# Performance work log

Hardware: AMD Instinct MI355X
Metric: run time of the kernel (lower is better)

Reference implementation:

```python
import jax, jax.numpy as jnp
import numpy as np

D_MODEL = 256
N_HEADS = 8
N_LEVELS = 4
N_POINTS = 4
SHAPES = [(128, 128), (64, 64), (32, 32), (16, 16)]  # (H, W) per level


def _query_hw(Lq):
    h = int(Lq ** 0.5)
    w = Lq // h
    if h * w != Lq:
        facs = [(i, Lq // i) for i in range(1, int(Lq ** 0.5) + 1) if Lq % i == 0]
        h, w = min(facs, key=lambda t: abs(t[0] - t[1]))
    return h, w


def _grid_sample(img, grid):
    # img: [B, D, H, W]; grid: [B, Lq, P, 2] in [-1,1] (x, y)
    # bilinear, padding_mode='zeros', align_corners=False
    B, D, H, W = img.shape
    gx, gy = grid[..., 0], grid[..., 1]
    x = ((gx + 1.0) * W - 1.0) * 0.5
    y = ((gy + 1.0) * H - 1.0) * 0.5
    x0 = jnp.floor(x)
    y0 = jnp.floor(y)
    wx1 = x - x0
    wy1 = y - y0
    wx0 = 1.0 - wx1
    wy0 = 1.0 - wy1
    x0i = x0.astype(jnp.int32)
    y0i = y0.astype(jnp.int32)
    x1i = x0i + 1
    y1i = y0i + 1
    img_flat = img.reshape(B, D, H * W)

    def gather(yi, xi):
        valid = (xi >= 0) & (xi < W) & (yi >= 0) & (yi < H)
        idx = jnp.clip(yi, 0, H - 1) * W + jnp.clip(xi, 0, W - 1)  # [B,Lq,P]
        v = jnp.take_along_axis(img_flat, idx.reshape(B, 1, -1), axis=2)
        v = v.reshape(B, D, *yi.shape[1:])  # [B,D,Lq,P]
        return v * valid[:, None].astype(img.dtype)

    return (gather(y0i, x0i) * (wy0 * wx0)[:, None]
            + gather(y0i, x1i) * (wy0 * wx1)[:, None]
            + gather(y1i, x0i) * (wy1 * wx0)[:, None]
            + gather(y1i, x1i) * (wy1 * wx1)[:, None])


def _forward(query, input_flatten, spatial_shapes,
             W_off, b_off, W_attn, b_attn, W_val, b_val, W_out, b_out):
    N, Lq, C = query.shape
    M, L, P = N_HEADS, N_LEVELS, N_POINTS
    D = C // M
    shapes = np.asarray(spatial_shapes)  # static

    value = (input_flatten @ W_val + b_val).reshape(N, -1, M, D)
    off = (query @ W_off + b_off).reshape(N, Lq, M, L, P, 2)
    attn = jax.nn.softmax((query @ W_attn + b_attn).reshape(N, Lq, M, L * P), axis=-1)
    attn = attn.reshape(N, Lq, M, L, P)

    # normalized reference grid derived from Len_q (2D branch)
    qh, qw = _query_hw(Lq)
    ry, rx = jnp.meshgrid(jnp.linspace(0.5, qh - 0.5, qh) / qh,
                          jnp.linspace(0.5, qw - 0.5, qw) / qw, indexing='ij')
    ref = jnp.stack([rx.reshape(-1), ry.reshape(-1)], axis=-1)  # [Lq, 2] (x,y)
    norm = jnp.asarray(np.stack([shapes[:, 1], shapes[:, 0]], -1), jnp.float32)  # [L,2]=(W,H)
    loc = ref[None, :, None, None, None, :] + off / norm[None, None, None, :, None, :]
    grids = 2.0 * loc - 1.0  # [N,Lq,M,L,P,2]

    starts = np.concatenate([[0], np.cumsum(shapes[:, 0] * shapes[:, 1])])
    sampled = []
    for l in range(L):
        H, W = int(shapes[l, 0]), int(shapes[l, 1])
        v = value[:, starts[l]:starts[l + 1]]            # [N, H*W, M, D]
        v = v.transpose(0, 2, 3, 1).reshape(N * M, D, H, W)
        g = grids[:, :, :, l].transpose(0, 2, 1, 3, 4).reshape(N * M, Lq, P, 2)
        sampled.append(_grid_sample(v, g))               # [NM, D, Lq, P]

    vals = jnp.stack(sampled, axis=-2)                   # [NM, D, Lq, L, P]
    # faithful to original: values flattened (P, L)-major, weights (L, P)-major
    vals = vals.transpose(0, 1, 2, 4, 3).reshape(N * M, D, Lq, P * L)
    w = attn.transpose(0, 2, 1, 3, 4).reshape(N * M, 1, Lq, L * P)
    out = (vals * w).sum(-1).reshape(N, M * D, Lq).transpose(0, 2, 1)  # [N,Lq,C]
    return out @ W_out + b_out


def setup_inputs():
    key = jax.random.key(0)
    ks = jax.random.split(key, 12)
    N, Lq, C = 2, 16384, D_MODEL
    M, L, P = N_HEADS, N_LEVELS, N_POINTS
    Lin = sum(h * w for h, w in SHAPES)
    s = 0.02
    # sampling_offsets bias: original directional grid init
    thetas = np.arange(M, dtype=np.float32) * (2.0 * np.pi / M)
    gi = np.stack([np.cos(thetas), np.sin(thetas)], -1)
    gi = gi / np.abs(gi).max(-1, keepdims=True)
    gi = np.tile(gi.reshape(M, 1, 1, 2), (1, L, P, 1))
    for i in range(P):
        gi[:, :, i, :] *= (i + 1)
    inp = {
        'query': jax.random.normal(ks[0], (N, Lq, C), jnp.float32),
        'reference_points': jax.random.uniform(ks[1], (N, Lq, L, 2), jnp.float32),
        'input_flatten': jax.random.normal(ks[2], (N, Lin, C), jnp.float32),
        'spatial_shapes': jnp.array(SHAPES, jnp.int32),
        'level_start_index': jnp.array(np.concatenate([[0], np.cumsum([h * w for h, w in SHAPES[:-1]])]), jnp.int32),
        'W_off': jax.random.normal(ks[3], (C, M * L * P * 2), jnp.float32) * s,
        'b_off': jnp.asarray(gi.reshape(-1), jnp.float32),
        'W_attn': jax.random.normal(ks[4], (C, M * L * P), jnp.float32) * s,
        'b_attn': jnp.zeros((M * L * P,), jnp.float32),
        'W_val': jax.random.normal(ks[5], (C, C), jnp.float32) * (1.0 / np.sqrt(C)),
        'b_val': jnp.zeros((C,), jnp.float32),
        'W_out': jax.random.normal(ks[6], (C, C), jnp.float32) * (1.0 / np.sqrt(C)),
        'b_out': jnp.zeros((C,), jnp.float32),
    }
    return inp


def reference(query, reference_points, input_flatten, spatial_shapes, level_start_index,
              W_off, b_off, W_attn, b_attn, W_val, b_val, W_out, b_out):
    assert reference_points.shape[-1] == 2
    return _forward(query, input_flatten, spatial_shapes,
                    W_off, b_off, W_attn, b_attn, W_val, b_val, W_out, b_out)
```

## Files before the change

kernel.cpp:

```cpp
#include <hip/hip_runtime.h>
#include <math.h>

#define NB   2
#define LQ   16384
#define CDIM 256
#define MH   8
#define DH   32
#define LIN  21760

typedef __attribute__((ext_vector_type(8))) _Float16 f16x8;
typedef __attribute__((ext_vector_type(4))) _Float16 f16x4;
typedef __attribute__((ext_vector_type(4))) float    f32x4;

__device__ __forceinline__ void async16(const void* g, void* l) {
    __builtin_amdgcn_global_load_lds(
        (const __attribute__((address_space(1))) void*)g,
        (__attribute__((address_space(3))) void*)l,
        16, 0, 0);
}

__global__ __launch_bounds__(256) void split_f16_kernel(
    const float* __restrict__ in, _Float16* __restrict__ o, int n8)
{
    const int i = blockIdx.x * 256 + threadIdx.x;
    if (i >= n8) return;
    const float4 v0 = ((const float4*)in)[i * 2];
    const float4 v1 = ((const float4*)in)[i * 2 + 1];
    f16x8 h;
    h[0] = (_Float16)v0.x; h[1] = (_Float16)v0.y;
    h[2] = (_Float16)v0.z; h[3] = (_Float16)v0.w;
    h[4] = (_Float16)v1.x; h[5] = (_Float16)v1.y;
    h[6] = (_Float16)v1.z; h[7] = (_Float16)v1.w;
    ((f16x8*)o)[i] = h;
}

__global__ __launch_bounds__(256) void tsplit_f16_kernel(
    const float* __restrict__ W, _Float16* __restrict__ t, int N)
{
    const int i = blockIdx.x * 256 + threadIdx.x;
    if (i >= N * 256) return;
    const int nn = i >> 8;
    const int kk = i & 255;
    t[i] = (_Float16)W[kk * N + nn];
}

template <bool OUT_F16>
__global__ __launch_bounds__(256) void gemm_f16(
    const _Float16* __restrict__ A, const _Float16* __restrict__ Bt,
    const float* __restrict__ bias0, const float* __restrict__ bias1,
    void* __restrict__ C0, void* __restrict__ C1,
    int M, int N, int K, int N0)
{
    __shared__ _Float16 Ash[128 * 32];
    __shared__ _Float16 Bsh[128 * 32];

    const int tid  = threadIdx.x;
    const int wave = tid >> 6, lane = tid & 63;
    const int quad = lane >> 4, l16 = lane & 15;
    const int bm = blockIdx.y * 128;
    const int bn = blockIdx.x * 128;
    const int wrow = wave * 32;

    f32x4 acc[2][8] = {};

    const int s0 = tid,        row0 = s0 >> 2, kg0 = (s0 & 3) << 3;
    const int s1 = tid + 256,  row1 = s1 >> 2, kg1 = (s1 & 3) << 3;

    for (int k0 = 0; k0 < K; k0 += 32) {
        async16(A  + (size_t)(bm + row0) * K + k0 + kg0, Ash + s0 * 8);
        async16(A  + (size_t)(bm + row1) * K + k0 + kg1, Ash + s1 * 8);
        async16(Bt + (size_t)(bn + row0) * K + k0 + kg0, Bsh + s0 * 8);
        async16(Bt + (size_t)(bn + row1) * K + k0 + kg1, Bsh + s1 * 8);
        __syncthreads();

        f16x8 ah[2];
        #pragma unroll
        for (int r = 0; r < 2; ++r)
            ah[r] = *(const f16x8*)&Ash[(wrow + r * 16 + l16) * 32 + quad * 8];
        #pragma unroll
        for (int half = 0; half < 2; ++half) {
            f16x8 bh[4];
            #pragma unroll
            for (int c = 0; c < 4; ++c)
                bh[c] = *(const f16x8*)&Bsh[(half * 64 + c * 16 + l16) * 32 + quad * 8];
            #pragma unroll
            for (int r = 0; r < 2; ++r)
                #pragma unroll
                for (int c = 0; c < 4; ++c)
                    acc[r][half * 4 + c] = __builtin_amdgcn_mfma_f32_16x16x32_f16(
                        ah[r], bh[c], acc[r][half * 4 + c], 0, 0, 0);
        }
        __syncthreads();
    }

    void* Cb; const float* bb; int ldc, coff;
    if (bn < N0) { Cb = C0; bb = bias0; ldc = N0;     coff = 0;  }
    else         { Cb = C1; bb = bias1; ldc = N - N0; coff = N0; }
    #pragma unroll
    for (int c = 0; c < 8; ++c) {
        const int col = bn + c * 16 + l16 - coff;
        const float bia = bb[col];
        #pragma unroll
        for (int r = 0; r < 2; ++r)
            #pragma unroll
            for (int i = 0; i < 4; ++i) {
                const int rr = bm + wrow + r * 16 + quad * 4 + i;
                const float v = acc[r][c][i] + bia;
                if (OUT_F16) ((_Float16*)Cb)[(size_t)rr * ldc + col] = (_Float16)v;
                else         ((float*)Cb)[(size_t)rr * ldc + col] = v;
            }
    }
}

__global__ __launch_bounds__(256) void softmax16_kernel(float* __restrict__ a, int rows)
{
    const int r = blockIdx.x * 256 + threadIdx.x;
    if (r >= rows) return;
    float* row = a + (size_t)r * 16;
    float v[16];
    float4* rv = (float4*)row;
    #pragma unroll
    for (int i = 0; i < 4; ++i) *(float4*)&v[i * 4] = rv[i];
    float mx = v[0];
    #pragma unroll
    for (int i = 1; i < 16; ++i) mx = fmaxf(mx, v[i]);
    float s = 0.f;
    #pragma unroll
    for (int i = 0; i < 16; ++i) { v[i] = __expf(v[i] - mx); s += v[i]; }
    const float inv = 1.f / s;
    #pragma unroll
    for (int i = 0; i < 16; ++i) v[i] *= inv;
    #pragma unroll
    for (int i = 0; i < 4; ++i) rv[i] = *(float4*)&v[i * 4];
}

__global__ __launch_bounds__(256) void sample_kernel_v7(
    const _Float16* __restrict__ value,
    const float* __restrict__ off,
    const float* __restrict__ attn,
    _Float16* __restrict__ outv)
{
    __shared__ __align__(16) float lds_task[8][516];

    const int tid = threadIdx.x;
    const int qbase = blockIdx.x * 4;

    #pragma unroll
    for (int j = 0; j < 2; ++j) {
        const int t  = tid + 256 * j;
        const int q  = t >> 7;
        const int m  = (t >> 4) & 7;
        const int pt = t & 15;
        const int l  = pt >> 2;
        const int p  = pt & 3;
        const int qi = qbase + q;
        const int lq = qi & (LQ - 1);
        const int n  = qi >> 14;

        const int Hl = 128 >> l;
        const int STARTS[4] = {0, 16384, 20480, 21504};

        const float2 oxy = *(const float2*)&off[(size_t)qi * 256 + m * 32 + pt * 2];
        const float w    = attn[(size_t)qi * 128 + m * 16 + p * 4 + l];

        const float refx = ((lq & 127) + 0.5f) * (1.0f / 128.0f);
        const float refy = ((lq >> 7)  + 0.5f) * (1.0f / 128.0f);

        const float x = refx * (float)Hl + oxy.x - 0.5f;
        const float y = refy * (float)Hl + oxy.y - 0.5f;
        const float x0f = floorf(x), y0f = floorf(y);
        const int x0 = (int)x0f, y0 = (int)y0f;
        const int x1 = x0 + 1,  y1 = y0 + 1;
        const float fx = x - x0f, fy = y - y0f;
        const float gx = 1.f - fx, gy = 1.f - fy;

        const float vx0 = (x0 >= 0 && x0 < Hl) ? 1.f : 0.f;
        const float vx1 = (x1 >= 0 && x1 < Hl) ? 1.f : 0.f;
        const float vy0 = (y0 >= 0 && y0 < Hl) ? 1.f : 0.f;
        const float vy1 = (y1 >= 0 && y1 < Hl) ? 1.f : 0.f;

        const int x0c = min(max(x0, 0), Hl - 1);
        const int x1c = min(max(x1, 0), Hl - 1);
        const int y0c = min(max(y0, 0), Hl - 1);
        const int y1c = min(max(y1, 0), Hl - 1);

        const int base = (n * LIN + STARTS[l]) * 256 + m * 32;
        const int i00 = base + (y0c * Hl + x0c) * 256;
        const int i01 = base + (y0c * Hl + x1c) * 256;
        const int i10 = base + (y1c * Hl + x0c) * 256;
        const int i11 = base + (y1c * Hl + x1c) * 256;

        float4 wv;
        wv.x = w * gy * gx * vy0 * vx0;
        wv.y = w * gy * fx * vy0 * vx1;
        wv.z = w * fy * gx * vy1 * vx0;
        wv.w = w * fy * fx * vy1 * vx1;

        float* dst = &lds_task[m][(q * 16 + pt) * 8];
        *(float4*)dst = wv;
        int4 iv = {i00, i01, i10, i11};
        *(int4*)(dst + 4) = iv;
    }
    __syncthreads();

    const int q  = tid >> 6;
    const int m  = (tid >> 3) & 7;
    const int d4 = tid & 7;
    const int qi = qbase + q;

    const _Float16* vbase = value + d4 * 4;

    float4 acc = {0.f, 0.f, 0.f, 0.f};
    #pragma unroll
    for (int pt = 0; pt < 16; ++pt) {
        const float* td = &lds_task[m][(q * 16 + pt) * 8];
        const float4 wv = *(const float4*)td;
        const int4  iv = *(const int4*)(td + 4);
        const f16x4 v00 = *(const f16x4*)&vbase[iv.x];
        const f16x4 v01 = *(const f16x4*)&vbase[iv.y];
        const f16x4 v10 = *(const f16x4*)&vbase[iv.z];
        const f16x4 v11 = *(const f16x4*)&vbase[iv.w];
        acc.x += wv.x * (float)v00[0] + wv.y * (float)v01[0] + wv.z * (float)v10[0] + wv.w * (float)v11[0];
        acc.y += wv.x * (float)v00[1] + wv.y * (float)v01[1] + wv.z * (float)v10[1] + wv.w * (float)v11[1];
        acc.z += wv.x * (float)v00[2] + wv.y * (float)v01[2] + wv.z * (float)v10[2] + wv.w * (float)v11[2];
        acc.w += wv.x * (float)v00[3] + wv.y * (float)v01[3] + wv.z * (float)v10[3] + wv.w * (float)v11[3];
    }

    f16x4 o;
    o.x = (_Float16)acc.x; o.y = (_Float16)acc.y;
    o.z = (_Float16)acc.z; o.w = (_Float16)acc.w;
    *(f16x4*)&outv[(size_t)qi * 256 + m * 32 + d4 * 4] = o;
}

extern "C" void kernel_launch(void* const* d_in, const int* in_sizes, int n_in,
                              void* d_out, int out_size, void* d_ws, size_t ws_size,
                              hipStream_t stream)
{
    const float* query         = (const float*)d_in[0];
    const float* input_flatten = (const float*)d_in[2];
    const float* W_off  = (const float*)d_in[5];
    const float* b_off  = (const float*)d_in[6];
    const float* W_attn = (const float*)d_in[7];
    const float* b_attn = (const float*)d_in[8];
    const float* W_val  = (const float*)d_in[9];
    const float* b_val  = (const float*)d_in[10];
    const float* W_out  = (const float*)d_in[11];
    const float* b_out  = (const float*)d_in[12];
    float* out = (float*)d_out;

    char* w = (char*)d_ws;
    _Float16* IFf16 = (_Float16*)w;
    _Float16* Qf16  = (_Float16*)w;
    _Float16* Sf16  = (_Float16*)w;
    _Float16* value16 = (_Float16*)(w + 23068672);
    float*    attnbuf = (float*)(w + 67633152);
    _Float16* Wvt = (_Float16*)(w + 84410368);
    _Float16* Wot = Wvt + 65536;
    _Float16* Wct = Wot + 65536;
    float* offbuf = out;

    dim3 blk(256);

    tsplit_f16_kernel<<<256, blk, 0, stream>>>(W_val, Wvt, 256);
    tsplit_f16_kernel<<<256, blk, 0, stream>>>(W_out, Wot, 256);
    tsplit_f16_kernel<<<256, blk, 0, stream>>>(W_off, Wct, 256);
    tsplit_f16_kernel<<<128, blk, 0, stream>>>(W_attn, Wct + 65536, 128);

    split_f16_kernel<<<(1392640 + 255) / 256, blk, 0, stream>>>(input_flatten, IFf16, 1392640);
    gemm_f16<true><<<dim3(2, 340), blk, 0, stream>>>(
        IFf16, Wvt, b_val, b_val, value16, value16, 43520, 256, 256, 256);

    split_f16_kernel<<<(1048576 + 255) / 256, blk, 0, stream>>>(query, Qf16, 1048576);
    gemm_f16<false><<<dim3(3, 256), blk, 0, stream>>>(
        Qf16, Wct, b_off, b_attn, offbuf, attnbuf, 32768, 384, 256, 256);

    softmax16_kernel<<<1024, blk, 0, stream>>>(attnbuf, 262144);

    sample_kernel_v7<<<8192, blk, 0, stream>>>(value16, offbuf, attnbuf, Sf16);

    gemm_f16<false><<<dim3(2, 256), blk, 0, stream>>>(
        Sf16, Wot, b_out, b_out, out, out, 32768, 256, 256, 256);
}
```

Baseline: 273.3 us.

## Fuse fp32-to-fp16 conversion into GEMMs, softmax into sampler, head-major value layout

The separate fp32-to-fp16 conversion kernels for input_flatten and query are removed. The GEMMs now load fp32 tiles into LDS asynchronously and convert them to fp16 in registers, which avoids a full extra read and write pass over both activations. The softmax kernel is folded into the sampler as 16-lane shuffle reductions, the four weight-transpose launches become one, and the value projection writes a head-major [head][pixel][32] layout so each head's gathers stay within a compact region. The costs are twice the LDS for the A tile, conversion work repeated in every column block, and strided 2-byte scattered stores in the value GEMM epilogue.

```diff
diff --git a/kernel.cpp b/kernel.cpp
--- a/kernel.cpp
+++ b/kernel.cpp
@@ -7,6 +7,7 @@
 #define MH   8
 #define DH   32
 #define LIN  21760
+#define NPIX (NB * LIN)
 
 typedef __attribute__((ext_vector_type(8))) _Float16 f16x8;
 typedef __attribute__((ext_vector_type(4))) _Float16 f16x4;
@@ -19,39 +20,36 @@
         16, 0, 0);
 }
 
-__global__ __launch_bounds__(256) void split_f16_kernel(
-    const float* __restrict__ in, _Float16* __restrict__ o, int n8)
+__global__ __launch_bounds__(256) void tsplit_all_kernel(
+    const float* __restrict__ Wv, const float* __restrict__ Wo,
+    const float* __restrict__ Wf, const float* __restrict__ Wa,
+    _Float16* __restrict__ Wvt, _Float16* __restrict__ Wot, _Float16* __restrict__ Wct)
 {
     const int i = blockIdx.x * 256 + threadIdx.x;
-    if (i >= n8) return;
-    const float4 v0 = ((const float4*)in)[i * 2];
-    const float4 v1 = ((const float4*)in)[i * 2 + 1];
-    f16x8 h;
-    h[0] = (_Float16)v0.x; h[1] = (_Float16)v0.y;
-    h[2] = (_Float16)v0.z; h[3] = (_Float16)v0.w;
-    h[4] = (_Float16)v1.x; h[5] = (_Float16)v1.y;
-    h[6] = (_Float16)v1.z; h[7] = (_Float16)v1.w;
-    ((f16x8*)o)[i] = h;
-}
-
-__global__ __launch_bounds__(256) void tsplit_f16_kernel(
-    const float* __restrict__ W, _Float16* __restrict__ t, int N)
-{
-    const int i = blockIdx.x * 256 + threadIdx.x;
-    if (i >= N * 256) return;
-    const int nn = i >> 8;
+    const int r = i >> 8;
     const int kk = i & 255;
-    t[i] = (_Float16)W[kk * N + nn];
-}
-
-template <bool OUT_F16>
+    if (r < 256) {
+        Wvt[r * 256 + kk] = (_Float16)Wv[kk * 256 + r];
+    } else if (r < 512) {
+        const int n = r - 256;
+        Wot[n * 256 + kk] = (_Float16)Wo[kk * 256 + n];
+    } else if (r < 768) {
+        const int n = r - 512;
+        Wct[n * 256 + kk] = (_Float16)Wf[kk * 256 + n];
+    } else {
+        const int n = r - 768;
+        Wct[(256 + n) * 256 + kk] = (_Float16)Wa[kk * 128 + n];
+    }
+}
+
+template <int OUT_MODE, bool A_F32>
 __global__ __launch_bounds__(256) void gemm_f16(
-    const _Float16* __restrict__ A, const _Float16* __restrict__ Bt,
+    const void* __restrict__ Araw, const _Float16* __restrict__ Bt,
     const float* __restrict__ bias0, const float* __restrict__ bias1,
     void* __restrict__ C0, void* __restrict__ C1,
     int M, int N, int K, int N0)
 {
-    __shared__ _Float16 Ash[128 * 32];
+    __shared__ __align__(16) char AshRaw[A_F32 ? 128 * 32 * 4 : 128 * 32 * 2];
     __shared__ _Float16 Bsh[128 * 32];
 
     const int tid  = threadIdx.x;
@@ -67,16 +65,44 @@
     const int s1 = tid + 256,  row1 = s1 >> 2, kg1 = (s1 & 3) << 3;
 
     for (int k0 = 0; k0 < K; k0 += 32) {
-        async16(A  + (size_t)(bm + row0) * K + k0 + kg0, Ash + s0 * 8);
-        async16(A  + (size_t)(bm + row1) * K + k0 + kg1, Ash + s1 * 8);
+        if (A_F32) {
+            const float* A = (const float*)Araw;
+            float* AshF = (float*)AshRaw;
+            #pragma unroll
+            for (int j = 0; j < 4; ++j) {
+                const int s = tid + 256 * j;
+                async16(A + (size_t)(bm + (s >> 3)) * K + k0 + ((s & 7) << 2),
+                        AshF + s * 4);
+            }
+        } else {
+            const _Float16* A = (const _Float16*)Araw;
+            _Float16* Ash = (_Float16*)AshRaw;
+            async16(A + (size_t)(bm + row0) * K + k0 + kg0, Ash + s0 * 8);
+            async16(A + (size_t)(bm + row1) * K + k0 + kg1, Ash + s1 * 8);
+        }
         async16(Bt + (size_t)(bn + row0) * K + k0 + kg0, Bsh + s0 * 8);
         async16(Bt + (size_t)(bn + row1) * K + k0 + kg1, Bsh + s1 * 8);
         __syncthreads();
 
         f16x8 ah[2];
         #pragma unroll
-        for (int r = 0; r < 2; ++r)
-            ah[r] = *(const f16x8*)&Ash[(wrow + r * 16 + l16) * 32 + quad * 8];
+        for (int r = 0; r < 2; ++r) {
+            if (A_F32) {
+                const float* AshF = (const float*)AshRaw;
+                const float* ap = &AshF[(wrow + r * 16 + l16) * 32 + quad * 8];
+                const f32x4 a0 = *(const f32x4*)ap;
+                const f32x4 a1 = *(const f32x4*)(ap + 4);
+                f16x8 h;
+                h[0] = (_Float16)a0[0]; h[1] = (_Float16)a0[1];
+                h[2] = (_Float16)a0[2]; h[3] = (_Float16)a0[3];
+                h[4] = (_Float16)a1[0]; h[5] = (_Float16)a1[1];
+                h[6] = (_Float16)a1[2]; h[7] = (_Float16)a1[3];
+                ah[r] = h;
+            } else {
+                const _Float16* Ash = (const _Float16*)AshRaw;
+                ah[r] = *(const f16x8*)&Ash[(wrow + r * 16 + l16) * 32 + quad * 8];
+            }
+        }
         #pragma unroll
         for (int half = 0; half < 2; ++half) {
             f16x8 bh[4];
@@ -106,35 +132,17 @@
             for (int i = 0; i < 4; ++i) {
                 const int rr = bm + wrow + r * 16 + quad * 4 + i;
                 const float v = acc[r][c][i] + bia;
-                if (OUT_F16) ((_Float16*)Cb)[(size_t)rr * ldc + col] = (_Float16)v;
-                else         ((float*)Cb)[(size_t)rr * ldc + col] = v;
+                if (OUT_MODE == 2)
+                    ((_Float16*)Cb)[((size_t)(col >> 5) * NPIX + rr) * 32 + (col & 31)] = (_Float16)v;
+                else if (OUT_MODE == 1)
+                    ((_Float16*)Cb)[(size_t)rr * ldc + col] = (_Float16)v;
+                else
+                    ((float*)Cb)[(size_t)rr * ldc + col] = v;
             }
     }
 }
 
-__global__ __launch_bounds__(256) void softmax16_kernel(float* __restrict__ a, int rows)
-{
-    const int r = blockIdx.x * 256 + threadIdx.x;
-    if (r >= rows) return;
-    float* row = a + (size_t)r * 16;
-    float v[16];
-    float4* rv = (float4*)row;
-    #pragma unroll
-    for (int i = 0; i < 4; ++i) *(float4*)&v[i * 4] = rv[i];
-    float mx = v[0];
-    #pragma unroll
-    for (int i = 1; i < 16; ++i) mx = fmaxf(mx, v[i]);
-    float s = 0.f;
-    #pragma unroll
-    for (int i = 0; i < 16; ++i) { v[i] = __expf(v[i] - mx); s += v[i]; }
-    const float inv = 1.f / s;
-    #pragma unroll
-    for (int i = 0; i < 16; ++i) v[i] *= inv;
-    #pragma unroll
-    for (int i = 0; i < 4; ++i) rv[i] = *(float4*)&v[i * 4];
-}
-
-__global__ __launch_bounds__(256) void sample_kernel_v7(
+__global__ __launch_bounds__(256) void sample_kernel_v8(
     const _Float16* __restrict__ value,
     const float* __restrict__ off,
     const float* __restrict__ attn,
@@ -161,7 +169,16 @@
         const int STARTS[4] = {0, 16384, 20480, 21504};
 
         const float2 oxy = *(const float2*)&off[(size_t)qi * 256 + m * 32 + pt * 2];
-        const float w    = attn[(size_t)qi * 128 + m * 16 + p * 4 + l];
+
+        const float logit = attn[(size_t)qi * 128 + m * 16 + p * 4 + l];
+        float mx = logit;
+        #pragma unroll
+        for (int d = 1; d < 16; d <<= 1) mx = fmaxf(mx, __shfl_xor(mx, d, 16));
+        const float e = __expf(logit - mx);
+        float sm = e;
+        #pragma unroll
+        for (int d = 1; d < 16; d <<= 1) sm += __shfl_xor(sm, d, 16);
+        const float w = e / sm;
 
         const float refx = ((lq & 127) + 0.5f) * (1.0f / 128.0f);
         const float refy = ((lq >> 7)  + 0.5f) * (1.0f / 128.0f);
@@ -184,11 +201,11 @@
         const int y0c = min(max(y0, 0), Hl - 1);
         const int y1c = min(max(y1, 0), Hl - 1);
 
-        const int base = (n * LIN + STARTS[l]) * 256 + m * 32;
-        const int i00 = base + (y0c * Hl + x0c) * 256;
-        const int i01 = base + (y0c * Hl + x1c) * 256;
-        const int i10 = base + (y1c * Hl + x0c) * 256;
-        const int i11 = base + (y1c * Hl + x1c) * 256;
+        const int base = m * (NPIX * 32) + (n * LIN + STARTS[l]) * 32;
+        const int i00 = base + (y0c * Hl + x0c) * 32;
+        const int i01 = base + (y0c * Hl + x1c) * 32;
+        const int i10 = base + (y1c * Hl + x0c) * 32;
+        const int i11 = base + (y1c * Hl + x1c) * 32;
 
         float4 wv;
         wv.x = w * gy * gx * vy0 * vx0;
@@ -249,9 +266,7 @@
     float* out = (float*)d_out;
 
     char* w = (char*)d_ws;
-    _Float16* IFf16 = (_Float16*)w;
-    _Float16* Qf16  = (_Float16*)w;
-    _Float16* Sf16  = (_Float16*)w;
+    _Float16* Sf16 = (_Float16*)w;
     _Float16* value16 = (_Float16*)(w + 23068672);
     float*    attnbuf = (float*)(w + 67633152);
     _Float16* Wvt = (_Float16*)(w + 84410368);
@@ -261,23 +276,16 @@
 
     dim3 blk(256);
 
-    tsplit_f16_kernel<<<256, blk, 0, stream>>>(W_val, Wvt, 256);
-    tsplit_f16_kernel<<<256, blk, 0, stream>>>(W_out, Wot, 256);
-    tsplit_f16_kernel<<<256, blk, 0, stream>>>(W_off, Wct, 256);
-    tsplit_f16_kernel<<<128, blk, 0, stream>>>(W_attn, Wct + 65536, 128);
-
-    split_f16_kernel<<<(1392640 + 255) / 256, blk, 0, stream>>>(input_flatten, IFf16, 1392640);
-    gemm_f16<true><<<dim3(2, 340), blk, 0, stream>>>(
-        IFf16, Wvt, b_val, b_val, value16, value16, 43520, 256, 256, 256);
-
-    split_f16_kernel<<<(1048576 + 255) / 256, blk, 0, stream>>>(query, Qf16, 1048576);
-    gemm_f16<false><<<dim3(3, 256), blk, 0, stream>>>(
-        Qf16, Wct, b_off, b_attn, offbuf, attnbuf, 32768, 384, 256, 256);
-
-    softmax16_kernel<<<1024, blk, 0, stream>>>(attnbuf, 262144);
-
-    sample_kernel_v7<<<8192, blk, 0, stream>>>(value16, offbuf, attnbuf, Sf16);
-
-    gemm_f16<false><<<dim3(2, 256), blk, 0, stream>>>(
+    tsplit_all_kernel<<<896, blk, 0, stream>>>(W_val, W_out, W_off, W_attn, Wvt, Wot, Wct);
+
+    gemm_f16<2, true><<<dim3(2, 340), blk, 0, stream>>>(
+        input_flatten, Wvt, b_val, b_val, value16, value16, 43520, 256, 256, 256);
+
+    gemm_f16<0, true><<<dim3(3, 256), blk, 0, stream>>>(
+        query, Wct, b_off, b_attn, offbuf, attnbuf, 32768, 384, 256, 256);
+
+    sample_kernel_v8<<<8192, blk, 0, stream>>>(value16, offbuf, attnbuf, Sf16);
+
+    gemm_f16<0, false><<<dim3(2, 256), blk, 0, stream>>>(
         Sf16, Wot, b_out, b_out, out, out, 32768, 256, 256, 256);
 }
```

Measured after the change: 254.0 us. 1.08x faster.
